# Kernel optimization log

Hardware: AMD Instinct MI355X
Metric: run time of the kernel (lower is better)

## Reference

```python
import jax, jax.numpy as jnp
import numpy as np

B, T, I, H = 32768, 200, 6, 6
FF, OUT = 128, 12


def setup_inputs() -> dict:
    key = jax.random.key(0)
    ks = jax.random.split(key, 10)
    s = lambda fan_in: 1.0 / np.sqrt(fan_in)
    inp = {
        "x": jax.random.normal(ks[0], (B, T, I), dtype=jnp.float32),
        # PyTorch LSTM params (gate order i, f, g, o)
        "W_ih": jax.random.uniform(ks[1], (4 * H, I), jnp.float32, -s(H), s(H)),
        "W_hh": jax.random.uniform(ks[2], (4 * H, H), jnp.float32, -s(H), s(H)),
        "b_ih": jax.random.uniform(ks[3], (4 * H,), jnp.float32, -s(H), s(H)),
        "b_hh": jax.random.uniform(ks[4], (4 * H,), jnp.float32, -s(H), s(H)),
        # MLP head (Dropout is identity in eval mode)
        "W1": jax.random.uniform(ks[5], (FF, T * H), jnp.float32, -s(T * H), s(T * H)),
        "b1": jax.random.uniform(ks[6], (FF,), jnp.float32, -s(T * H), s(T * H)),
        "W2": jax.random.uniform(ks[7], (OUT, FF), jnp.float32, -s(FF), s(FF)),
        "b2": jax.random.uniform(ks[8], (OUT,), jnp.float32, -s(FF), s(FF)),
    }
    return inp


def _lstm(x, W_ih, W_hh, b_ih, b_hh):
    # x: [B, T, I] -> hidden sequence [B, T, H]
    # Precompute input projections for all timesteps at once: [T, B, 4H]
    xg = jnp.einsum("bti,gi->tbg", x, W_ih) + (b_ih + b_hh)
    h0 = jnp.zeros((x.shape[0], H), x.dtype)
    c0 = jnp.zeros((x.shape[0], H), x.dtype)

    def step(carry, xg_t):
        h, c = carry
        gates = xg_t + h @ W_hh.T  # [B, 4H]
        i, f, g, o = jnp.split(gates, 4, axis=-1)
        i = jax.nn.sigmoid(i)
        f = jax.nn.sigmoid(f)
        g = jnp.tanh(g)
        o = jax.nn.sigmoid(o)
        c = f * c + i * g
        h = o * jnp.tanh(c)
        return (h, c), h

    _, hs = jax.lax.scan(step, (h0, c0), xg)  # hs: [T, B, H]
    return jnp.transpose(hs, (1, 0, 2))  # [B, T, H]


def reference(x, W_ih, W_hh, b_ih, b_hh, W1, b1, W2, b2):
    hs = _lstm(x, W_ih, W_hh, b_ih, b_hh)          # [B, T, H]
    flat = hs.reshape(hs.shape[0], -1)             # [B, T*H]
    hid = jax.nn.relu(flat @ W1.T + b1)            # [B, 128]
    return hid @ W2.T + b2                         # [B, 12]
```

## Files before the change

### kernel.cpp

```cpp
#include <hip/hip_runtime.h>
#include <hip/hip_bf16.h>

#define Bn   32768
#define Tn   200
#define In   6
#define Hn   6
#define FFn  128
#define OUTn 12
#define KP   1600

typedef __attribute__((ext_vector_type(2))) float          f32x2;
typedef __attribute__((ext_vector_type(4))) float          f32x4;
typedef __attribute__((ext_vector_type(8))) short          bf16x8;
typedef __attribute__((ext_vector_type(8))) unsigned short u16x8;
typedef __attribute__((ext_vector_type(4))) unsigned int   u32x4;

#define LOG2E 1.442695041f

__device__ __forceinline__ f32x2 pkfma(f32x2 a, f32x2 b, f32x2 c) {
#if __has_builtin(__builtin_elementwise_fma)
    return __builtin_elementwise_fma(a, b, c);
#else
    return a * b + c;
#endif
}
__device__ __forceinline__ float swap1(float v) {
    return __int_as_float(__builtin_amdgcn_mov_dpp(__float_as_int(v), 0xB1, 0xF, 0xF, true));
}
__device__ __forceinline__ unsigned short f2bf(float v) {
    unsigned u = __float_as_uint(v);
    unsigned r = u + 0x7FFFu + ((u >> 16) & 1u);
    return (unsigned short)(r >> 16);
}
__device__ __forceinline__ unsigned cvt_pk_bf16(float a, float b) {
    unsigned r;
    asm("v_cvt_pk_bf16_f32 %0, %1, %2" : "=v"(r) : "v"(a), "v"(b));
    return r;
}

#define BAR() do {                                          \
    asm volatile("s_waitcnt lgkmcnt(0)" ::: "memory");      \
    __builtin_amdgcn_sched_barrier(0);                      \
    __builtin_amdgcn_s_barrier();                           \
    __builtin_amdgcn_sched_barrier(0);                      \
} while (0)

__global__ void prep_kernel(const float* __restrict__ W1, unsigned short* __restrict__ W1p) {
    int idx = blockIdx.x * 256 + threadIdx.x;
    if (idx >= FFn * KP) return;
    int ff = idx / KP, kp = idx - ff * KP;
    int t = kp >> 3, p = kp & 7;
    float v = 0.f;
    if (p != 3 && p != 7) {
        int h = (p < 3) ? p : (p - 1);
        v = W1[ff * (Tn * Hn) + t * Hn + h];
    }
    W1p[idx] = f2bf(v);
}

__global__ __launch_bounds__(512, 2)
void fused_kernel(const float* __restrict__ x,
                  const float* __restrict__ W_ih, const float* __restrict__ W_hh,
                  const float* __restrict__ b_ih, const float* __restrict__ b_hh,
                  const unsigned short* __restrict__ W1p,
                  const float* __restrict__ b1,
                  const float* __restrict__ W2, const float* __restrict__ b2,
                  float* __restrict__ out)
{
    __shared__ float          htile32[2][8][128][8];
    __shared__ unsigned short hidS[128][136];
    __shared__ float          W2s[OUTn * FFn];

    const int tid = threadIdx.x;
    const int wv  = tid >> 6;
    const int b0  = blockIdx.x * 128;

    if (wv < 4) {
        const int sloc = tid >> 1;
        const int role = tid & 1;

        f32x2 Wx[6][6], Wh[6][6], bias2[6];
        #pragma unroll
        for (int gt = 0; gt < 4; ++gt) {
            #pragma unroll
            for (int m = 0; m < 3; ++m) {
                const int j = gt * 3 + m;
                const int p = j >> 1, hf = j & 1;
                const int row = gt * 6 + role * 3 + m;
                const float sc = (gt == 2) ? (2.f * LOG2E) : (-LOG2E);
                #pragma unroll
                for (int k = 0; k < 6; ++k) Wx[p][k][hf] = sc * W_ih[row * 6 + k];
                #pragma unroll
                for (int k = 0; k < 3; ++k) Wh[p][k][hf]     = sc * W_hh[row * 6 + role * 3 + k];
                #pragma unroll
                for (int k = 0; k < 3; ++k) Wh[p][3 + k][hf] = sc * W_hh[row * 6 + (1 - role) * 3 + k];
                bias2[p][hf] = sc * (b_ih[row] + b_hh[row]);
            }
        }

        float hOwn[3] = {0.f, 0.f, 0.f}, hOth[3] = {0.f, 0.f, 0.f}, cS[3] = {0.f, 0.f, 0.f};

        const f32x4* xb4 = (const f32x4*)(x + (size_t)(b0 + sloc) * (Tn * In));

        auto STEPS4 = [&](const f32x4 (&bx)[6], int slot, int sbase) {
            #pragma unroll
            for (int s = 0; s < 4; ++s) {
                float xv[6];
                #pragma unroll
                for (int k = 0; k < 6; ++k) { const int fl = s * 6 + k; xv[k] = bx[fl >> 2][fl & 3]; }
                f32x2 a2[6];
                #pragma unroll
                for (int p = 0; p < 6; ++p) a2[p] = bias2[p];
                #pragma unroll
                for (int k = 0; k < 6; ++k) {
                    const f32x2 xs = (f32x2){xv[k], xv[k]};
                    #pragma unroll
                    for (int p = 0; p < 6; ++p) a2[p] = pkfma(Wx[p][k], xs, a2[p]);
                }
                #pragma unroll
                for (int k = 0; k < 3; ++k) {
                    const f32x2 hs = (f32x2){hOwn[k], hOwn[k]};
                    #pragma unroll
                    for (int p = 0; p < 6; ++p) a2[p] = pkfma(Wh[p][k], hs, a2[p]);
                }
                #pragma unroll
                for (int k = 0; k < 3; ++k) {
                    const f32x2 hs = (f32x2){hOth[k], hOth[k]};
                    #pragma unroll
                    for (int p = 0; p < 6; ++p) a2[p] = pkfma(Wh[p][3 + k], hs, a2[p]);
                }
                float av[12];
                #pragma unroll
                for (int p = 0; p < 6; ++p) { av[2 * p] = a2[p][0]; av[2 * p + 1] = a2[p][1]; }

                float hq[3];
                #pragma unroll
                for (int m = 0; m < 3; ++m) {
                    const float Ei = __builtin_amdgcn_exp2f(av[m]);
                    const float Ef = __builtin_amdgcn_exp2f(av[3 + m]);
                    const float Eg = __builtin_amdgcn_exp2f(av[6 + m]);
                    const float Eo = __builtin_amdgcn_exp2f(av[9 + m]);
                    const float fv = __builtin_amdgcn_rcpf(1.f + Ef);
                    const float ig = (Eg - 1.f) *
                                     __builtin_amdgcn_rcpf((1.f + Ei) * (1.f + Eg));
                    const float c  = fmaf(fv, cS[m], ig);
                    cS[m] = c;
                    const float Ec = __builtin_amdgcn_exp2f(fminf(2.f * LOG2E * c, 60.f));
                    const float hv = (Ec - 1.f) *
                                     __builtin_amdgcn_rcpf((1.f + Eo) * (1.f + Ec));
                    hOwn[m] = hv;
                    hOth[m] = swap1(hv);
                    hq[m]   = hv;
                }
                const f32x4 hw4 = (f32x4){hq[0], hq[1], hq[2], 0.f};
                *((f32x4*)&htile32[slot][sbase + s][sloc][role * 4]) = hw4;
            }
        };

        f32x4 bufA[6], bufB[6];
        #pragma unroll
        for (int q = 0; q < 6; ++q) bufA[q] = xb4[q];

        for (int g = 0; g < 25; ++g) {
            #pragma unroll
            for (int q = 0; q < 6; ++q) bufB[q] = xb4[(2 * g + 1) * 6 + q];
            STEPS4(bufA, g & 1, 0);
            if (g < 24) {
                #pragma unroll
                for (int q = 0; q < 6; ++q) bufA[q] = xb4[(2 * g + 2) * 6 + q];
            }
            STEPS4(bufB, g & 1, 4);
            BAR();
        }
        for (int q = tid; q < OUTn * FFn; q += 256) W2s[q] = W2[q];

    } else {
        const int wv2 = wv - 4;
        const int l   = tid & 63;
        const int lr  = l & 15;
        const int lg  = l >> 4;

        const unsigned short* wrow[2];
        #pragma unroll
        for (int n = 0; n < 2; ++n) wrow[n] = W1p + (size_t)(wv2 * 32 + n * 16 + lr) * KP;

        f32x4 acc[8][2];
        #pragma unroll
        for (int m = 0; m < 8; ++m)
            #pragma unroll
            for (int n = 0; n < 2; ++n)
                acc[m][n] = (f32x4){0.f, 0.f, 0.f, 0.f};

        auto LOADB = [&](int g, bf16x8 (&bf)[2][2]) {
            #pragma unroll
            for (int kc = 0; kc < 2; ++kc)
                #pragma unroll
                for (int n = 0; n < 2; ++n)
                    bf[kc][n] = *((const bf16x8*)&wrow[n][g * 64 + kc * 32 + lg * 8]);
        };

        auto MFMAG8 = [&](int slot, const bf16x8 (&bf)[2][2]) {
            #pragma unroll
            for (int kc = 0; kc < 2; ++kc) {
                bf16x8 af[8];
                #pragma unroll
                for (int m = 0; m < 8; ++m) {
                    const f32x4 lo = *((const f32x4*)&htile32[slot][kc * 4 + lg][m * 16 + lr][0]);
                    const f32x4 hi = *((const f32x4*)&htile32[slot][kc * 4 + lg][m * 16 + lr][4]);
                    u32x4 w;
                    w[0] = cvt_pk_bf16(lo[0], lo[1]);
                    w[1] = cvt_pk_bf16(lo[2], lo[3]);
                    w[2] = cvt_pk_bf16(hi[0], hi[1]);
                    w[3] = cvt_pk_bf16(hi[2], hi[3]);
                    af[m] = *((const bf16x8*)&w);
                }
                #pragma unroll
                for (int n = 0; n < 2; ++n)
                    #pragma unroll
                    for (int m = 0; m < 8; ++m)
                        acc[m][n] = __builtin_amdgcn_mfma_f32_16x16x32_bf16(af[m], bf[kc][n], acc[m][n], 0, 0, 0);
            }
        };

        bf16x8 bfA[2][2], bfB[2][2];
        LOADB(0, bfA);
        for (int gg = 0; gg < 12; ++gg) {
            BAR();
            LOADB(2 * gg + 1, bfB);
            MFMAG8(0, bfA);
            BAR();
            const int gn = (2 * gg + 2 < 25) ? (2 * gg + 2) : 24;
            LOADB(gn, bfA);
            MFMAG8(1, bfB);
        }
        BAR();
        MFMAG8(0, bfA);

        float b1v[2];
        #pragma unroll
        for (int n = 0; n < 2; ++n) b1v[n] = b1[wv2 * 32 + n * 16 + lr];
        #pragma unroll
        for (int m = 0; m < 8; ++m)
            #pragma unroll
            for (int n = 0; n < 2; ++n)
                #pragma unroll
                for (int r = 0; r < 4; ++r)
                    hidS[m * 16 + lg * 4 + r][wv2 * 32 + n * 16 + lr] =
                        f2bf(fmaxf(acc[m][n][r] + b1v[n], 0.f));
    }

    __syncthreads();

    const int s2 = tid >> 2;
    const int q  = tid & 3;
    float oa[3];
    #pragma unroll
    for (int jj = 0; jj < 3; ++jj) oa[jj] = b2[q * 3 + jj];
    for (int k8 = 0; k8 < 16; ++k8) {
        const u16x8 hv8 = *((const u16x8*)&hidS[s2][k8 * 8]);
        #pragma unroll
        for (int e = 0; e < 8; ++e) {
            const float hv = __uint_as_float(((unsigned)(unsigned short)hv8[e]) << 16);
            const int k = k8 * 8 + e;
            #pragma unroll
            for (int jj = 0; jj < 3; ++jj)
                oa[jj] = fmaf(hv, W2s[(q * 3 + jj) * FFn + k], oa[jj]);
        }
    }
    float* op = out + (size_t)(b0 + s2) * OUTn + q * 3;
    #pragma unroll
    for (int jj = 0; jj < 3; ++jj) op[jj] = oa[jj];
}

extern "C" void kernel_launch(void* const* d_in, const int* in_sizes, int n_in,
                              void* d_out, int out_size, void* d_ws, size_t ws_size,
                              hipStream_t stream) {
    const float* x    = (const float*)d_in[0];
    const float* W_ih = (const float*)d_in[1];
    const float* W_hh = (const float*)d_in[2];
    const float* b_ih = (const float*)d_in[3];
    const float* b_hh = (const float*)d_in[4];
    const float* W1   = (const float*)d_in[5];
    const float* b1   = (const float*)d_in[6];
    const float* W2   = (const float*)d_in[7];
    const float* b2   = (const float*)d_in[8];
    unsigned short* W1p = (unsigned short*)d_ws;
    float* out = (float*)d_out;

    prep_kernel<<<(FFn * KP + 255) / 256, 256, 0, stream>>>(W1, W1p);
    fused_kernel<<<Bn / 128, 512, 0, stream>>>(x, W_ih, W_hh, b_ih, b_hh,
                                               W1p, b1, W2, b2, out);
}
```

Measured before the change: 126.5 us.

## Halve block batch to 64 and store LSTM hidden states as bf16 in LDS

Each block now handles 64 sequences with 256 threads instead of 128 with 512. That means 2 LSTM waves and 2 MFMA waves, and each MFMA wave covers 64 FF columns with 4x4 accumulator tiles. The recurrence writes h converted to bf16 directly into a half-size shared tile, so the MFMA waves no longer load fp32 and convert per fragment. This doubles the block count and cuts LDS traffic and size, which may raise occupancy. The cost is that each W1 tile is reloaded by twice as many blocks, and the B-fragment loads per wave double.

New measurement: 142.3 us. 12.5% more time.

```diff
diff --git a/kernel.cpp b/kernel.cpp
--- a/kernel.cpp
+++ b/kernel.cpp
@@ -8,12 +8,13 @@
 #define FFn  128
 #define OUTn 12
 #define KP   1600
+#define SB   64
 
 typedef __attribute__((ext_vector_type(2))) float          f32x2;
 typedef __attribute__((ext_vector_type(4))) float          f32x4;
 typedef __attribute__((ext_vector_type(8))) short          bf16x8;
+typedef __attribute__((ext_vector_type(4))) unsigned short u16x4;
 typedef __attribute__((ext_vector_type(8))) unsigned short u16x8;
-typedef __attribute__((ext_vector_type(4))) unsigned int   u32x4;
 
 #define LOG2E 1.442695041f
 
@@ -31,11 +32,6 @@
     unsigned u = __float_as_uint(v);
     unsigned r = u + 0x7FFFu + ((u >> 16) & 1u);
     return (unsigned short)(r >> 16);
-}
-__device__ __forceinline__ unsigned cvt_pk_bf16(float a, float b) {
-    unsigned r;
-    asm("v_cvt_pk_bf16_f32 %0, %1, %2" : "=v"(r) : "v"(a), "v"(b));
-    return r;
 }
 
 #define BAR() do {                                          \
@@ -58,7 +54,7 @@
     W1p[idx] = f2bf(v);
 }
 
-__global__ __launch_bounds__(512, 2)
+__global__ __launch_bounds__(256, 2)
 void fused_kernel(const float* __restrict__ x,
                   const float* __restrict__ W_ih, const float* __restrict__ W_hh,
                   const float* __restrict__ b_ih, const float* __restrict__ b_hh,
@@ -67,15 +63,15 @@
                   const float* __restrict__ W2, const float* __restrict__ b2,
                   float* __restrict__ out)
 {
-    __shared__ float          htile32[2][8][128][8];
-    __shared__ unsigned short hidS[128][136];
+    __shared__ unsigned short htile[2][8][SB][8];
+    __shared__ unsigned short hidS[SB][136];
     __shared__ float          W2s[OUTn * FFn];
 
     const int tid = threadIdx.x;
     const int wv  = tid >> 6;
-    const int b0  = blockIdx.x * 128;
-
-    if (wv < 4) {
+    const int b0  = blockIdx.x * SB;
+
+    if (wv < 2) {
         const int sloc = tid >> 1;
         const int role = tid & 1;
 
@@ -133,7 +129,7 @@
                 #pragma unroll
                 for (int p = 0; p < 6; ++p) { av[2 * p] = a2[p][0]; av[2 * p + 1] = a2[p][1]; }
 
-                float hq[3];
+                unsigned short hb[3];
                 #pragma unroll
                 for (int m = 0; m < 3; ++m) {
                     const float Ei = __builtin_amdgcn_exp2f(av[m]);
@@ -150,10 +146,10 @@
                                      __builtin_amdgcn_rcpf((1.f + Eo) * (1.f + Ec));
                     hOwn[m] = hv;
                     hOth[m] = swap1(hv);
-                    hq[m]   = hv;
-                }
-                const f32x4 hw4 = (f32x4){hq[0], hq[1], hq[2], 0.f};
-                *((f32x4*)&htile32[slot][sbase + s][sloc][role * 4]) = hw4;
+                    hb[m]   = f2bf(hv);
+                }
+                u16x4 hw; hw.x = hb[0]; hw.y = hb[1]; hw.z = hb[2]; hw.w = 0;
+                *((u16x4*)&htile[slot][sbase + s][sloc][role * 4]) = hw;
             }
         };
 
@@ -172,57 +168,49 @@
             STEPS4(bufB, g & 1, 4);
             BAR();
         }
-        for (int q = tid; q < OUTn * FFn; q += 256) W2s[q] = W2[q];
+        for (int q = tid; q < OUTn * FFn; q += 128) W2s[q] = W2[q];
 
     } else {
-        const int wv2 = wv - 4;
+        const int wv2 = wv - 2;
         const int l   = tid & 63;
         const int lr  = l & 15;
         const int lg  = l >> 4;
 
-        const unsigned short* wrow[2];
-        #pragma unroll
-        for (int n = 0; n < 2; ++n) wrow[n] = W1p + (size_t)(wv2 * 32 + n * 16 + lr) * KP;
-
-        f32x4 acc[8][2];
-        #pragma unroll
-        for (int m = 0; m < 8; ++m)
-            #pragma unroll
-            for (int n = 0; n < 2; ++n)
+        const unsigned short* wrow[4];
+        #pragma unroll
+        for (int n = 0; n < 4; ++n) wrow[n] = W1p + (size_t)(wv2 * 64 + n * 16 + lr) * KP;
+
+        f32x4 acc[4][4];
+        #pragma unroll
+        for (int m = 0; m < 4; ++m)
+            #pragma unroll
+            for (int n = 0; n < 4; ++n)
                 acc[m][n] = (f32x4){0.f, 0.f, 0.f, 0.f};
 
-        auto LOADB = [&](int g, bf16x8 (&bf)[2][2]) {
+        auto LOADB = [&](int g, bf16x8 (&bf)[2][4]) {
             #pragma unroll
             for (int kc = 0; kc < 2; ++kc)
                 #pragma unroll
-                for (int n = 0; n < 2; ++n)
+                for (int n = 0; n < 4; ++n)
                     bf[kc][n] = *((const bf16x8*)&wrow[n][g * 64 + kc * 32 + lg * 8]);
         };
 
-        auto MFMAG8 = [&](int slot, const bf16x8 (&bf)[2][2]) {
+        auto MFMAG8 = [&](int slot, const bf16x8 (&bf)[2][4]) {
             #pragma unroll
             for (int kc = 0; kc < 2; ++kc) {
-                bf16x8 af[8];
-                #pragma unroll
-                for (int m = 0; m < 8; ++m) {
-                    const f32x4 lo = *((const f32x4*)&htile32[slot][kc * 4 + lg][m * 16 + lr][0]);
-                    const f32x4 hi = *((const f32x4*)&htile32[slot][kc * 4 + lg][m * 16 + lr][4]);
-                    u32x4 w;
-                    w[0] = cvt_pk_bf16(lo[0], lo[1]);
-                    w[1] = cvt_pk_bf16(lo[2], lo[3]);
-                    w[2] = cvt_pk_bf16(hi[0], hi[1]);
-                    w[3] = cvt_pk_bf16(hi[2], hi[3]);
-                    af[m] = *((const bf16x8*)&w);
-                }
-                #pragma unroll
-                for (int n = 0; n < 2; ++n)
-                    #pragma unroll
-                    for (int m = 0; m < 8; ++m)
+                bf16x8 af[4];
+                #pragma unroll
+                for (int m = 0; m < 4; ++m)
+                    af[m] = *((const bf16x8*)&htile[slot][kc * 4 + lg][m * 16 + lr][0]);
+                #pragma unroll
+                for (int n = 0; n < 4; ++n)
+                    #pragma unroll
+                    for (int m = 0; m < 4; ++m)
                         acc[m][n] = __builtin_amdgcn_mfma_f32_16x16x32_bf16(af[m], bf[kc][n], acc[m][n], 0, 0, 0);
             }
         };
 
-        bf16x8 bfA[2][2], bfB[2][2];
+        bf16x8 bfA[2][4], bfB[2][4];
         LOADB(0, bfA);
         for (int gg = 0; gg < 12; ++gg) {
             BAR();
@@ -236,16 +224,16 @@
         BAR();
         MFMAG8(0, bfA);
 
-        float b1v[2];
-        #pragma unroll
-        for (int n = 0; n < 2; ++n) b1v[n] = b1[wv2 * 32 + n * 16 + lr];
-        #pragma unroll
-        for (int m = 0; m < 8; ++m)
-            #pragma unroll
-            for (int n = 0; n < 2; ++n)
+        float b1v[4];
+        #pragma unroll
+        for (int n = 0; n < 4; ++n) b1v[n] = b1[wv2 * 64 + n * 16 + lr];
+        #pragma unroll
+        for (int m = 0; m < 4; ++m)
+            #pragma unroll
+            for (int n = 0; n < 4; ++n)
                 #pragma unroll
                 for (int r = 0; r < 4; ++r)
-                    hidS[m * 16 + lg * 4 + r][wv2 * 32 + n * 16 + lr] =
+                    hidS[m * 16 + lg * 4 + r][wv2 * 64 + n * 16 + lr] =
                         f2bf(fmaxf(acc[m][n][r] + b1v[n], 0.f));
     }
 
@@ -288,6 +276,6 @@
     float* out = (float*)d_out;
 
     prep_kernel<<<(FFn * KP + 255) / 256, 256, 0, stream>>>(W1, W1p);
-    fused_kernel<<<Bn / 128, 512, 0, stream>>>(x, W_ih, W_hh, b_ih, b_hh,
-                                               W1p, b1, W2, b2, out);
-}
+    fused_kernel<<<Bn / SB, 256, 0, stream>>>(x, W_ih, W_hh, b_ih, b_hh,
+                                              W1p, b1, W2, b2, out);
+}
```
